# Kernel optimization log

Measured on AMD Instinct MI355X. Metric: run time of the kernel, lower is better.

## Reference

```python
import jax, jax.numpy as jnp
import numpy as np

TWO_PI = 2.0 * np.pi
P = 3      # AR order
KMAX = 5   # winding offsets per side
D = 3      # torus dimension

def setup_inputs() -> dict:
    key = jax.random.key(0)
    kg, kphi = jax.random.split(key)
    g = jax.random.normal(kg, (32, 16, 2048, D), dtype=jnp.float32)  # (n_mc, n_samples, T, d) angles
    ar_phi = 0.1 * jax.random.normal(kphi, (D, P), dtype=jnp.float32)
    ar_eta = 0.05 * jnp.ones((D,), dtype=jnp.float32)
    ar_c = jnp.zeros((D,), dtype=jnp.float32)
    return {"g": g, "ar_phi": ar_phi, "ar_eta": ar_eta, "ar_c": ar_c}

def _logmap(x):
    # Torus logmap: wrap to (-pi, pi]
    return jnp.mod(x + np.pi, TWO_PI) - np.pi

def reference(g, ar_phi, ar_eta, ar_c):
    # prms: (ar_c, ar_phi, ar_eta**2); scale = sqrt(eta)
    scale = jnp.sqrt(jnp.square(ar_eta))  # (d,) == |ar_eta|
    # Torus: inverse(g) = -g, gmul = add
    dg = g[..., 1:, :] - g[..., :-1, :]
    dx = _logmap(dg)                       # (..., T-1, d)
    Td = dx.shape[-2]
    # AR history stack: (..., T', d, p), T' = T-1-p
    hist = jnp.stack([dx[..., P - j - 1:Td - j - 1, :] for j in range(P)], axis=-1)
    dy = dx[..., P:, :] - (ar_phi * hist).sum(-1)  # (..., T', d)
    ks = jnp.arange(-KMAX, KMAX + 1, dtype=dy.dtype)
    z = dy[..., :, None] + TWO_PI * ks             # (..., T', d, K)
    log_scale = jnp.log(scale)
    lp = (-0.5 * jnp.square((z - ar_c[:, None]) / scale[:, None])
          - log_scale[:, None]
          - 0.5 * jnp.log(jnp.asarray(TWO_PI, dy.dtype)))
    # Faithful to the diagonal branch of ARP.forward: per-dim log_q with d=1
    # logsumexp's over a size-1 axis (identity) then .sum(-1) over the K
    # winding offsets, i.e. the winding log-probs are SUMMED (not logsumexp'd),
    # then summed over dims j.
    lq = lp.sum(-1).sum(-1)                # (..., T')
    return lq.sum(-1).sum(-1)              # (n_mc,)
```

## Files before the change

### kernel.cpp

```cpp
#include <hip/hip_runtime.h>
#include <math.h>

#define T 2048
#define D 3
#define P 3
#define NK 11
#define SUM_K2 110.0f
#define TWO_PI_F 6.28318530717958647692f
#define INV_TWO_PI_F 0.15915494309189533577f
#define PI_F 3.14159265358979323846f

#define SPLIT 4
#define SEG 511

__device__ __forceinline__ float wrap_pi(float x) {
    float k = rintf(x * INV_TWO_PI_F);
    return fmaf(-k, TWO_PI_F, x);
}

__global__ __launch_bounds__(256) void arp_kernel(
    const float* __restrict__ g,
    const float* __restrict__ ar_phi,
    const float* __restrict__ ar_eta,
    const float* __restrict__ ar_c,
    float* __restrict__ partial,
    float* __restrict__ out,
    int n_samples,
    int use_ws)
{
    __shared__ float sg[SEG * 3 + 12 + 4];
    __shared__ float sdx[(SEG + 3) * 3];
    __shared__ float wave_sums[4];

    const int blk    = blockIdx.x;
    const int series = blk >> 2;
    const int seg    = blk & (SPLIT - 1);
    const int tid    = threadIdx.x;

    const int t0      = seg * SEG;
    const int start_f = t0 * 3;
    const int a0      = start_f & ~3;
    const int ofs     = start_f - a0;
    const int nfloat  = SEG * 3 + 12 + ofs;
    const int nvec    = (nfloat + 3) >> 2;

    {
        const float4* src = (const float4*)(g + (size_t)series * (T * D) + a0);
        float4* dst = (float4*)sg;
        for (int i = tid; i < nvec; i += 256) dst[i] = src[i];
    }
    __syncthreads();

    {
        const int n = (SEG + 3) * 3;
        for (int f = tid; f < n; f += 256)
            sdx[f] = wrap_pi(sg[ofs + f + 3] - sg[ofs + f]);
    }
    __syncthreads();

    float ph[D][P], inv_s2[D], cc[D];
    float Cd_sum = 0.0f;
    #pragma unroll
    for (int d = 0; d < D; ++d) {
        float s = fabsf(ar_eta[d]);
        inv_s2[d] = 1.0f / (s * s);
        cc[d] = ar_c[d];
        #pragma unroll
        for (int j = 0; j < P; ++j) ph[d][j] = ar_phi[d * P + j];
        Cd_sum += -0.5f * inv_s2[d] * (4.0f * PI_F * PI_F * SUM_K2)
                  - (float)NK * logf(s)
                  - 0.5f * (float)NK * logf(TWO_PI_F);
    }

    float acc = 0.0f;
    for (int t = tid; t < SEG; t += 256) {
        float w[12];
        #pragma unroll
        for (int m = 0; m < 12; ++m) w[m] = sdx[t * 3 + m];
        #pragma unroll
        for (int d = 0; d < D; ++d) {
            float dy = w[9 + d] - (ph[d][0] * w[6 + d]
                                 + ph[d][1] * w[3 + d]
                                 + ph[d][2] * w[d]);
            float z = dy - cc[d];
            acc += -0.5f * (float)NK * z * z * inv_s2[d];
        }
    }

    #pragma unroll
    for (int off = 32; off > 0; off >>= 1) acc += __shfl_down(acc, off, 64);
    const int wave = tid >> 6, lane = tid & 63;
    if (lane == 0) wave_sums[wave] = acc;
    __syncthreads();
    if (tid == 0) {
        float block_sum = wave_sums[0] + wave_sums[1] + wave_sums[2] + wave_sums[3];
        block_sum += (float)SEG * Cd_sum;
        if (use_ws) {
            partial[blk] = block_sum;
        } else {
            const int mc = series / n_samples;
            atomicAdd(&out[mc], block_sum);
        }
    }
}

__global__ __launch_bounds__(64) void reduce_kernel(
    const float* __restrict__ partial,
    float* __restrict__ out,
    int per_mc)
{
    const int mc = blockIdx.x;
    float v = 0.0f;
    for (int i = threadIdx.x; i < per_mc; i += 64)
        v += partial[(size_t)mc * per_mc + i];
    #pragma unroll
    for (int off = 32; off > 0; off >>= 1) v += __shfl_down(v, off, 64);
    if (threadIdx.x == 0) out[mc] = v;
}

extern "C" void kernel_launch(void* const* d_in, const int* in_sizes, int n_in,
                              void* d_out, int out_size, void* d_ws, size_t ws_size,
                              hipStream_t stream) {
    const float* g      = (const float*)d_in[0];
    const float* ar_phi = (const float*)d_in[1];
    const float* ar_eta = (const float*)d_in[2];
    const float* ar_c   = (const float*)d_in[3];
    float* out = (float*)d_out;

    const int n_series  = in_sizes[0] / (T * D);
    const int n_mc      = out_size;
    const int n_samples = n_series / n_mc;
    const int n_blocks  = n_series * SPLIT;
    const int per_mc    = n_samples * SPLIT;

    const int use_ws = (d_ws != nullptr &&
                        ws_size >= (size_t)n_blocks * sizeof(float)) ? 1 : 0;
    float* partial = (float*)d_ws;

    if (!use_ws) {
        hipMemsetAsync(out, 0, (size_t)out_size * sizeof(float), stream);
    }
    arp_kernel<<<n_blocks, 256, 0, stream>>>(g, ar_phi, ar_eta, ar_c,
                                             partial, out, n_samples, use_ws);
    if (use_ws)
        reduce_kernel<<<n_mc, 64, 0, stream>>>(partial, out, per_mc);
}
```

Before: 70.62 us.

## Drop LDS staging and compute four outputs per thread from direct vector loads

The shared-memory staging of raw angles and wrapped differences is removed. Each thread now loads six float4 values straight from global memory and computes four consecutive AR residual terms in registers. Each series is covered by two blocks of 1024 outputs instead of four segments. This removes two block barriers and the LDS round trips. In exchange, neighbouring threads load overlapping windows and the wrap is recomputed for those overlaps, relying on cache to absorb the duplicate reads.

Measured after the change: 68.58 us (median of 2 runs). -2.9%, faster.

```diff
diff --git a/kernel.cpp b/kernel.cpp
--- a/kernel.cpp
+++ b/kernel.cpp
@@ -10,8 +10,10 @@
 #define INV_TWO_PI_F 0.15915494309189533577f
 #define PI_F 3.14159265358979323846f
 
-#define SPLIT 4
-#define SEG 511
+#define TP (T - 1 - P)
+#define OUT_PER_THREAD 4
+#define OUT_PER_BLOCK 1024
+#define BLOCKS_PER_SERIES 2
 
 __device__ __forceinline__ float wrap_pi(float x) {
     float k = rintf(x * INV_TWO_PI_F);
@@ -28,35 +30,13 @@
     int n_samples,
     int use_ws)
 {
-    __shared__ float sg[SEG * 3 + 12 + 4];
-    __shared__ float sdx[(SEG + 3) * 3];
     __shared__ float wave_sums[4];
 
     const int blk    = blockIdx.x;
-    const int series = blk >> 2;
-    const int seg    = blk & (SPLIT - 1);
+    const int series = blk >> 1;
+    const int half   = blk & 1;
     const int tid    = threadIdx.x;
-
-    const int t0      = seg * SEG;
-    const int start_f = t0 * 3;
-    const int a0      = start_f & ~3;
-    const int ofs     = start_f - a0;
-    const int nfloat  = SEG * 3 + 12 + ofs;
-    const int nvec    = (nfloat + 3) >> 2;
-
-    {
-        const float4* src = (const float4*)(g + (size_t)series * (T * D) + a0);
-        float4* dst = (float4*)sg;
-        for (int i = tid; i < nvec; i += 256) dst[i] = src[i];
-    }
-    __syncthreads();
-
-    {
-        const int n = (SEG + 3) * 3;
-        for (int f = tid; f < n; f += 256)
-            sdx[f] = wrap_pi(sg[ofs + f + 3] - sg[ofs + f]);
-    }
-    __syncthreads();
+    const int t      = half * OUT_PER_BLOCK + tid * OUT_PER_THREAD;
 
     float ph[D][P], inv_s2[D], cc[D];
     float Cd_sum = 0.0f;
@@ -73,18 +53,37 @@
     }
 
     float acc = 0.0f;
-    for (int t = tid; t < SEG; t += 256) {
-        float w[12];
+    if (t < TP) {
+        const float4* src4 = (const float4*)(g + (size_t)series * (T * D) + t * 3);
+        float4 q[6];
         #pragma unroll
-        for (int m = 0; m < 12; ++m) w[m] = sdx[t * 3 + m];
+        for (int m = 0; m < 6; ++m) q[m] = src4[m];
+
+        float vv[24];
         #pragma unroll
-        for (int d = 0; d < D; ++d) {
-            float dy = w[9 + d] - (ph[d][0] * w[6 + d]
-                                 + ph[d][1] * w[3 + d]
-                                 + ph[d][2] * w[d]);
-            float z = dy - cc[d];
-            acc += -0.5f * (float)NK * z * z * inv_s2[d];
+        for (int m = 0; m < 6; ++m) {
+            vv[4 * m + 0] = q[m].x;  vv[4 * m + 1] = q[m].y;
+            vv[4 * m + 2] = q[m].z;  vv[4 * m + 3] = q[m].w;
         }
+
+        float dxv[21];
+        #pragma unroll
+        for (int m = 0; m < 21; ++m) dxv[m] = wrap_pi(vv[m + 3] - vv[m]);
+
+        float q2 = 0.0f;
+        #pragma unroll
+        for (int k = 0; k < 4; ++k) {
+            #pragma unroll
+            for (int d = 0; d < D; ++d) {
+                float dy = dxv[(k + 3) * 3 + d]
+                         - (ph[d][0] * dxv[(k + 2) * 3 + d]
+                          + ph[d][1] * dxv[(k + 1) * 3 + d]
+                          + ph[d][2] * dxv[k * 3 + d]);
+                float z = dy - cc[d];
+                q2 = fmaf(z * z, inv_s2[d], q2);
+            }
+        }
+        acc = -0.5f * (float)NK * q2;
     }
 
     #pragma unroll
@@ -94,7 +93,9 @@
     __syncthreads();
     if (tid == 0) {
         float block_sum = wave_sums[0] + wave_sums[1] + wave_sums[2] + wave_sums[3];
-        block_sum += (float)SEG * Cd_sum;
+        int cnt = TP - half * OUT_PER_BLOCK;
+        if (cnt > OUT_PER_BLOCK) cnt = OUT_PER_BLOCK;
+        block_sum += (float)cnt * Cd_sum;
         if (use_ws) {
             partial[blk] = block_sum;
         } else {
@@ -130,8 +131,8 @@
     const int n_series  = in_sizes[0] / (T * D);
     const int n_mc      = out_size;
     const int n_samples = n_series / n_mc;
-    const int n_blocks  = n_series * SPLIT;
-    const int per_mc    = n_samples * SPLIT;
+    const int n_blocks  = n_series * BLOCKS_PER_SERIES;
+    const int per_mc    = n_samples * BLOCKS_PER_SERIES;
 
     const int use_ws = (d_ws != nullptr &&
                         ws_size >= (size_t)n_blocks * sizeof(float)) ? 1 : 0;
```
